# Kernel tuning notes

Hardware: AMD Instinct MI355X
Metric: run time of the kernel (lower is better)

The kernel has to match this reference:

```python
import jax, jax.numpy as jnp
import numpy as np

N_NODES = 50000
N_EDGES = 1600000
IN_F = 512
OUT_F = 256


def setup_inputs() -> dict:
    key = jax.random.key(0)
    k1, k2, k3, k4, k5 = jax.random.split(key, 5)
    features = jax.random.normal(k1, (N_NODES, IN_F), dtype=jnp.float32)
    # xavier_uniform init for weight [in_features, out_features]
    limit = np.sqrt(6.0 / (IN_F + OUT_F)).astype(np.float32)
    weight = jax.random.uniform(k2, (IN_F, OUT_F), dtype=jnp.float32,
                                minval=-limit, maxval=limit)
    # COO sparse adjacency (normalized edge weights in [0,1))
    edge_vals = jax.random.uniform(k3, (N_EDGES,), dtype=jnp.float32)
    edge_rows = jax.random.randint(k4, (N_EDGES,), 0, N_NODES, dtype=jnp.int32)
    edge_cols = jax.random.randint(k5, (N_EDGES,), 0, N_NODES, dtype=jnp.int32)
    return {"features": features, "weight": weight, "edge_vals": edge_vals,
            "edge_rows": edge_rows, "edge_cols": edge_cols}


def reference(features, weight, edge_vals, edge_rows, edge_cols):
    # dropout p=0.0 / eval mode -> identity
    support = features @ weight                      # [N, out_f] dense GEMM
    # torch.spmm(adj, support): out[r] += val * support[c] for each edge (r, c)
    gathered = support[edge_cols] * edge_vals[:, None]   # [E, out_f]
    output = jax.ops.segment_sum(gathered, edge_rows, num_segments=N_NODES)
    return jax.nn.relu(output)
```

## Files before the change

### kernel.cpp

```cpp
#include <hip/hip_runtime.h>

#define N_NODES 50000
#define N_EDGES 1600000
#define IN_F    512
#define OUT_F   256

#define BROWS   128
#define NBINS   ((N_NODES + BROWS - 1) / BROWS)
#define BATCH   2048
#define NBATCHES ((N_EDGES + BATCH - 1) / BATCH)

typedef __attribute__((ext_vector_type(8))) short bf16x8;
typedef __attribute__((ext_vector_type(4))) float f32x4;

__device__ __forceinline__ short bf16rne(float f) {
    unsigned u = __builtin_bit_cast(unsigned, f);
    u += 0x7fffu + ((u >> 16) & 1u);
    return (short)(u >> 16);
}

__device__ __forceinline__ float b2f(unsigned short h) {
    unsigned u = (unsigned)h << 16;
    return __builtin_bit_cast(float, u);
}

__global__ __launch_bounds__(256) void wt_kernel(const float* __restrict__ W,
                                                 short* __restrict__ Wt) {
    int idx = blockIdx.x * 256 + threadIdx.x;
    if (idx < IN_F * OUT_F) {
        int n = idx >> 9;
        int k = idx & 511;
        Wt[idx] = bf16rne(W[(size_t)k * OUT_F + n]);
    }
}

#define ASTRIDE 40
#define BSTRIDE 40

__global__ __launch_bounds__(256) void gemm_mfma_kernel(const float* __restrict__ A,
                                                        const short* __restrict__ Wt,
                                                        unsigned short* __restrict__ Cb) {
    __shared__ short As[64 * ASTRIDE];
    __shared__ short Bs[256 * BSTRIDE];

    const int tid  = threadIdx.x;
    const int wave = tid >> 6;
    const int lane = tid & 63;
    const int m0   = blockIdx.x * 64;
    const int n0w  = wave * 64;

    const int quad = lane >> 4;
    const int l16  = lane & 15;

    const int ar = tid >> 2;
    const int aq = tid & 3;

    f32x4 zero4 = {0.f, 0.f, 0.f, 0.f};
    f32x4 acc[4][4];
#pragma unroll
    for (int i = 0; i < 4; ++i)
#pragma unroll
        for (int j = 0; j < 4; ++j) acc[i][j] = zero4;

    for (int k0 = 0; k0 < IN_F; k0 += 32) {
        {
            const int gm = m0 + ar;
            float4 v0 = make_float4(0.f, 0.f, 0.f, 0.f);
            float4 v1 = v0;
            if (gm < N_NODES) {
                const float* p = A + (size_t)gm * IN_F + k0 + aq * 8;
                v0 = *(const float4*)p;
                v1 = *(const float4*)(p + 4);
            }
            bf16x8 b;
            b[0] = bf16rne(v0.x); b[1] = bf16rne(v0.y);
            b[2] = bf16rne(v0.z); b[3] = bf16rne(v0.w);
            b[4] = bf16rne(v1.x); b[5] = bf16rne(v1.y);
            b[6] = bf16rne(v1.z); b[7] = bf16rne(v1.w);
            *(bf16x8*)&As[ar * ASTRIDE + aq * 8] = b;
        }
        {
            const short* src = Wt + (size_t)tid * IN_F + k0;
            bf16x8 w0 = *(const bf16x8*)(src + 0);
            bf16x8 w1 = *(const bf16x8*)(src + 8);
            bf16x8 w2 = *(const bf16x8*)(src + 16);
            bf16x8 w3 = *(const bf16x8*)(src + 24);
            short* dst = &Bs[tid * BSTRIDE];
            *(bf16x8*)(dst + 0)  = w0;
            *(bf16x8*)(dst + 8)  = w1;
            *(bf16x8*)(dst + 16) = w2;
            *(bf16x8*)(dst + 24) = w3;
        }
        __syncthreads();

        bf16x8 af[4], bf[4];
#pragma unroll
        for (int mt = 0; mt < 4; ++mt)
            af[mt] = *(const bf16x8*)&As[(mt * 16 + l16) * ASTRIDE + quad * 8];
#pragma unroll
        for (int nt = 0; nt < 4; ++nt)
            bf[nt] = *(const bf16x8*)&Bs[(n0w + nt * 16 + l16) * BSTRIDE + quad * 8];

#pragma unroll
        for (int mt = 0; mt < 4; ++mt)
#pragma unroll
            for (int nt = 0; nt < 4; ++nt)
                acc[mt][nt] = __builtin_amdgcn_mfma_f32_16x16x32_bf16(
                    af[mt], bf[nt], acc[mt][nt], 0, 0, 0);
        __syncthreads();
    }

#pragma unroll
    for (int mt = 0; mt < 4; ++mt) {
        const int rbase = m0 + mt * 16 + quad * 4;
#pragma unroll
        for (int i = 0; i < 4; ++i) {
            const int row = rbase + i;
            if (row < N_NODES) {
#pragma unroll
                for (int nt = 0; nt < 4; ++nt)
                    Cb[(size_t)row * OUT_F + n0w + nt * 16 + l16] =
                        (unsigned short)bf16rne(acc[mt][nt][i]);
            }
        }
    }
}

__global__ __launch_bounds__(256) void zero_bins_kernel(int* __restrict__ binCounts) {
    int i = blockIdx.x * 256 + threadIdx.x;
    if (i < NBINS) binCounts[i] = 0;
}

__global__ __launch_bounds__(256) void histA_kernel(const int* __restrict__ rows,
                                                    int* __restrict__ binCounts) {
    __shared__ int lh[NBINS];
    const int tid = threadIdx.x;
    for (int i = tid; i < NBINS; i += 256) lh[i] = 0;
    __syncthreads();
    for (int i = blockIdx.x * 256 + tid; i < N_EDGES; i += gridDim.x * 256)
        atomicAdd(&lh[rows[i] >> 7], 1);
    __syncthreads();
    for (int i = tid; i < NBINS; i += 256)
        if (lh[i]) atomicAdd(&binCounts[i], lh[i]);
}

__global__ __launch_bounds__(256) void scanA_kernel(const int* __restrict__ binCounts,
                                                    int* __restrict__ binStart,
                                                    int* __restrict__ gcursor) {
    __shared__ int stmp[256];
    const int tid = threadIdx.x;
    const int i0 = 2 * tid, i1 = 2 * tid + 1;
    const int a0 = (i0 < NBINS) ? binCounts[i0] : 0;
    const int a1 = (i1 < NBINS) ? binCounts[i1] : 0;
    const int pair = a0 + a1;
    stmp[tid] = pair;
    for (int off = 1; off < 256; off <<= 1) {
        __syncthreads();
        int t = (tid >= off) ? stmp[tid - off] : 0;
        __syncthreads();
        stmp[tid] += t;
    }
    __syncthreads();
    const int pexcl = stmp[tid] - pair;
    if (i0 < NBINS) { binStart[i0] = pexcl;      gcursor[i0] = pexcl; }
    if (i1 < NBINS) { binStart[i1] = pexcl + a0; gcursor[i1] = pexcl + a0; }
}

__global__ __launch_bounds__(256) void fillA_kernel(const int* __restrict__ rows,
                                                    const int* __restrict__ cols,
                                                    const float* __restrict__ vals,
                                                    int* __restrict__ gcursor,
                                                    int2* __restrict__ binned) {
    __shared__ int lhist[NBINS];
    __shared__ int lexcl[NBINS];
    __shared__ int gbase[NBINS];
    __shared__ int stmp[256];
    __shared__ int2 lstage[BATCH];
    __shared__ unsigned short sbucket[BATCH];

    const int tid   = threadIdx.x;
    const int start = blockIdx.x * BATCH;
    const int count = min(BATCH, N_EDGES - start);

    for (int i = tid; i < NBINS; i += 256) lhist[i] = 0;
    __syncthreads();

    int myrow[8], myrank[8];
#pragma unroll
    for (int j = 0; j < 8; ++j) {
        const int s = j * 256 + tid;
        if (s < count) {
            const int r = rows[start + s];
            myrow[j]  = r;
            myrank[j] = atomicAdd(&lhist[r >> 7], 1);
        }
    }
    __syncthreads();

    {
        const int i0 = 2 * tid, i1 = 2 * tid + 1;
        const int a0 = (i0 < NBINS) ? lhist[i0] : 0;
        const int a1 = (i1 < NBINS) ? lhist[i1] : 0;
        const int pair = a0 + a1;
        stmp[tid] = pair;
        for (int off = 1; off < 256; off <<= 1) {
            __syncthreads();
            int t = (tid >= off) ? stmp[tid - off] : 0;
            __syncthreads();
            stmp[tid] += t;
        }
        __syncthreads();
        const int pexcl = stmp[tid] - pair;
        if (i0 < NBINS) {
            lexcl[i0] = pexcl;
            gbase[i0] = a0 ? atomicAdd(&gcursor[i0], a0) : 0;
        }
        if (i1 < NBINS) {
            lexcl[i1] = pexcl + a0;
            gbase[i1] = a1 ? atomicAdd(&gcursor[i1], a1) : 0;
        }
    }
    __syncthreads();

#pragma unroll
    for (int j = 0; j < 8; ++j) {
        const int s = j * 256 + tid;
        if (s < count) {
            const int r   = myrow[j];
            const int b   = r >> 7;
            const int pos = lexcl[b] + myrank[j];
            lstage[pos]  = make_int2(((r & 127) << 16) | cols[start + s],
                                     __float_as_int(vals[start + s]));
            sbucket[pos] = (unsigned short)b;
        }
    }
    __syncthreads();

#pragma unroll
    for (int j = 0; j < 8; ++j) {
        const int s = j * 256 + tid;
        if (s < count) {
            const int b = sbucket[s];
            binned[gbase[b] + (s - lexcl[b])] = lstage[s];
        }
    }
}

__global__ __launch_bounds__(256) void sortB_kernel(const int2* __restrict__ binned,
                                                    const int* __restrict__ binStart,
                                                    const int* __restrict__ binCounts,
                                                    int* __restrict__ excl,
                                                    unsigned int* __restrict__ ecv) {
    __shared__ int lhist[BROWS];
    __shared__ int lcur[BROWS];

    const int tid  = threadIdx.x;
    const int b    = blockIdx.x;
    const int base = binStart[b];
    const int cnt  = binCounts[b];

    if (tid < BROWS) lhist[tid] = 0;
    __syncthreads();

    for (int i = tid; i < cnt; i += 256)
        atomicAdd(&lhist[binned[base + i].x >> 16], 1);
    __syncthreads();

    if (tid < BROWS) lcur[tid] = lhist[tid];
    for (int off = 1; off < BROWS; off <<= 1) {
        __syncthreads();
        int t = (tid >= off && tid < BROWS) ? lcur[tid - off] : 0;
        __syncthreads();
        if (tid < BROWS) lcur[tid] += t;
    }
    __syncthreads();
    if (tid < BROWS) {
        const int pexcl = lcur[tid] - lhist[tid];
        const int row   = b * BROWS + tid;
        lcur[tid] = pexcl;
        if (row < N_NODES) excl[row] = base + pexcl;
    }
    __syncthreads();

    for (int i = tid; i < cnt; i += 256) {
        const int2 e  = binned[base + i];
        const int rl  = e.x >> 16;
        const int col = e.x & 0xFFFF;
        const int rank = atomicAdd(&lcur[rl], 1);
        ecv[base + rank] = ((unsigned int)col << 16) |
                           (unsigned short)bf16rne(__int_as_float(e.y));
    }
}

__global__ __launch_bounds__(256) void gather_kernel(const ushort4* __restrict__ support,
                                                     const int* __restrict__ excl,
                                                     const unsigned int* __restrict__ ecv,
                                                     float4* __restrict__ out) {
    const int tid  = threadIdx.x;
    const int row  = blockIdx.x * 4 + (tid >> 6);
    const int lane = tid & 63;
    if (row >= N_NODES) return;

    const int start = excl[row];
    const int end   = (row + 1 < N_NODES) ? excl[row + 1] : N_EDGES;

    float4 acc = make_float4(0.f, 0.f, 0.f, 0.f);
    int e = start;
    const int end4 = start + ((end - start) & ~3);
    for (; e < end4; e += 4) {
        const unsigned int p0 = ecv[e];
        const unsigned int p1 = ecv[e + 1];
        const unsigned int p2 = ecv[e + 2];
        const unsigned int p3 = ecv[e + 3];
        const ushort4 s0 = support[(size_t)(p0 >> 16) * 64 + lane];
        const ushort4 s1 = support[(size_t)(p1 >> 16) * 64 + lane];
        const ushort4 s2 = support[(size_t)(p2 >> 16) * 64 + lane];
        const ushort4 s3 = support[(size_t)(p3 >> 16) * 64 + lane];
        const float v0 = b2f((unsigned short)(p0 & 0xFFFF));
        const float v1 = b2f((unsigned short)(p1 & 0xFFFF));
        const float v2 = b2f((unsigned short)(p2 & 0xFFFF));
        const float v3 = b2f((unsigned short)(p3 & 0xFFFF));
        acc.x += v0 * b2f(s0.x); acc.y += v0 * b2f(s0.y);
        acc.z += v0 * b2f(s0.z); acc.w += v0 * b2f(s0.w);
        acc.x += v1 * b2f(s1.x); acc.y += v1 * b2f(s1.y);
        acc.z += v1 * b2f(s1.z); acc.w += v1 * b2f(s1.w);
        acc.x += v2 * b2f(s2.x); acc.y += v2 * b2f(s2.y);
        acc.z += v2 * b2f(s2.z); acc.w += v2 * b2f(s2.w);
        acc.x += v3 * b2f(s3.x); acc.y += v3 * b2f(s3.y);
        acc.z += v3 * b2f(s3.z); acc.w += v3 * b2f(s3.w);
    }
    for (; e < end; ++e) {
        const unsigned int p0 = ecv[e];
        const ushort4 s0 = support[(size_t)(p0 >> 16) * 64 + lane];
        const float v0 = b2f((unsigned short)(p0 & 0xFFFF));
        acc.x += v0 * b2f(s0.x); acc.y += v0 * b2f(s0.y);
        acc.z += v0 * b2f(s0.z); acc.w += v0 * b2f(s0.w);
    }

    acc.x = fmaxf(acc.x, 0.f);
    acc.y = fmaxf(acc.y, 0.f);
    acc.z = fmaxf(acc.z, 0.f);
    acc.w = fmaxf(acc.w, 0.f);
    out[(size_t)row * 64 + lane] = acc;
}

extern "C" void kernel_launch(void* const* d_in, const int* in_sizes, int n_in,
                              void* d_out, int out_size, void* d_ws, size_t ws_size,
                              hipStream_t stream) {
    const float* features  = (const float*)d_in[0];
    const float* weight    = (const float*)d_in[1];
    const float* edge_vals = (const float*)d_in[2];
    const int*   edge_rows = (const int*)d_in[3];
    const int*   edge_cols = (const int*)d_in[4];
    float* out = (float*)d_out;

    unsigned short* support_bf = (unsigned short*)d_ws;
    int2*  binned    = (int2*)(support_bf + (size_t)N_NODES * OUT_F);
    unsigned int* ecv = (unsigned int*)(binned + N_EDGES);
    int*   excl      = (int*)(ecv + N_EDGES);
    int*   binCounts = excl + N_NODES;
    int*   binStart  = binCounts + 512;
    int*   gcursor   = binStart + 512;
    short* Wt        = (short*)(gcursor + 512);

    wt_kernel<<<(IN_F * OUT_F + 255) / 256, 256, 0, stream>>>(weight, Wt);

    gemm_mfma_kernel<<<(N_NODES + 63) / 64, 256, 0, stream>>>(features, Wt, support_bf);

    zero_bins_kernel<<<2, 256, 0, stream>>>(binCounts);
    histA_kernel<<<256, 256, 0, stream>>>(edge_rows, binCounts);
    scanA_kernel<<<1, 256, 0, stream>>>(binCounts, binStart, gcursor);
    fillA_kernel<<<NBATCHES, 256, 0, stream>>>(edge_rows, edge_cols, edge_vals,
                                               gcursor, binned);
    sortB_kernel<<<NBINS, 256, 0, stream>>>(binned, binStart, binCounts, excl, ecv);

    gather_kernel<<<(N_NODES + 3) / 4, 256, 0, stream>>>(
        (const ushort4*)support_bf, excl, ecv, (float4*)out);
}
```

Measured before the change: 388.2 us.

## Enlarge GEMM block to 128 rows with 8 waves and split gather launch

The GEMM kernel now uses 512 threads and 128-row tiles, arranged as a 2x4 grid of waves. Each tile of the transposed weight loaded into shared memory is therefore reused across twice as many feature rows, which halves the weight traffic per output row. Separately, the gather kernel takes a row offset and is launched twice over the two halves of the nodes, which adds a launch without any clear benefit. The larger block and its shared memory use could lower occupancy.

```diff
diff --git a/kernel.cpp b/kernel.cpp
--- a/kernel.cpp
+++ b/kernel.cpp
@@ -37,23 +37,27 @@
 #define ASTRIDE 40
 #define BSTRIDE 40
 
-__global__ __launch_bounds__(256) void gemm_mfma_kernel(const float* __restrict__ A,
+__global__ __launch_bounds__(512) void gemm_mfma_kernel(const float* __restrict__ A,
                                                         const short* __restrict__ Wt,
                                                         unsigned short* __restrict__ Cb) {
-    __shared__ short As[64 * ASTRIDE];
+    __shared__ short As[128 * ASTRIDE];
     __shared__ short Bs[256 * BSTRIDE];
 
     const int tid  = threadIdx.x;
     const int wave = tid >> 6;
     const int lane = tid & 63;
-    const int m0   = blockIdx.x * 64;
-    const int n0w  = wave * 64;
+    const int m0   = blockIdx.x * 128;
+    const int wrow = (wave >> 2) * 64;
+    const int wcol = (wave & 3) * 64;
 
     const int quad = lane >> 4;
     const int l16  = lane & 15;
 
     const int ar = tid >> 2;
     const int aq = tid & 3;
+
+    const int bn = tid >> 1;
+    const int bh = tid & 1;
 
     f32x4 zero4 = {0.f, 0.f, 0.f, 0.f};
     f32x4 acc[4][4];
@@ -80,26 +84,22 @@
             *(bf16x8*)&As[ar * ASTRIDE + aq * 8] = b;
         }
         {
-            const short* src = Wt + (size_t)tid * IN_F + k0;
+            const short* src = Wt + (size_t)bn * IN_F + k0 + bh * 16;
             bf16x8 w0 = *(const bf16x8*)(src + 0);
             bf16x8 w1 = *(const bf16x8*)(src + 8);
-            bf16x8 w2 = *(const bf16x8*)(src + 16);
-            bf16x8 w3 = *(const bf16x8*)(src + 24);
-            short* dst = &Bs[tid * BSTRIDE];
-            *(bf16x8*)(dst + 0)  = w0;
-            *(bf16x8*)(dst + 8)  = w1;
-            *(bf16x8*)(dst + 16) = w2;
-            *(bf16x8*)(dst + 24) = w3;
+            short* dst = &Bs[bn * BSTRIDE + bh * 16];
+            *(bf16x8*)(dst + 0) = w0;
+            *(bf16x8*)(dst + 8) = w1;
         }
         __syncthreads();
 
         bf16x8 af[4], bf[4];
 #pragma unroll
         for (int mt = 0; mt < 4; ++mt)
-            af[mt] = *(const bf16x8*)&As[(mt * 16 + l16) * ASTRIDE + quad * 8];
+            af[mt] = *(const bf16x8*)&As[(wrow + mt * 16 + l16) * ASTRIDE + quad * 8];
 #pragma unroll
         for (int nt = 0; nt < 4; ++nt)
-            bf[nt] = *(const bf16x8*)&Bs[(n0w + nt * 16 + l16) * BSTRIDE + quad * 8];
+            bf[nt] = *(const bf16x8*)&Bs[(wcol + nt * 16 + l16) * BSTRIDE + quad * 8];
 
 #pragma unroll
         for (int mt = 0; mt < 4; ++mt)
@@ -112,14 +112,14 @@
 
 #pragma unroll
     for (int mt = 0; mt < 4; ++mt) {
-        const int rbase = m0 + mt * 16 + quad * 4;
+        const int rbase = m0 + wrow + mt * 16 + quad * 4;
 #pragma unroll
         for (int i = 0; i < 4; ++i) {
             const int row = rbase + i;
             if (row < N_NODES) {
 #pragma unroll
                 for (int nt = 0; nt < 4; ++nt)
-                    Cb[(size_t)row * OUT_F + n0w + nt * 16 + l16] =
+                    Cb[(size_t)row * OUT_F + wcol + nt * 16 + l16] =
                         (unsigned short)bf16rne(acc[mt][nt][i]);
             }
         }
@@ -295,9 +295,10 @@
 __global__ __launch_bounds__(256) void gather_kernel(const ushort4* __restrict__ support,
                                                      const int* __restrict__ excl,
                                                      const unsigned int* __restrict__ ecv,
-                                                     float4* __restrict__ out) {
+                                                     float4* __restrict__ out,
+                                                     int row0) {
     const int tid  = threadIdx.x;
-    const int row  = blockIdx.x * 4 + (tid >> 6);
+    const int row  = row0 + blockIdx.x * 4 + (tid >> 6);
     const int lane = tid & 63;
     if (row >= N_NODES) return;
 
@@ -365,7 +366,7 @@
 
     wt_kernel<<<(IN_F * OUT_F + 255) / 256, 256, 0, stream>>>(weight, Wt);
 
-    gemm_mfma_kernel<<<(N_NODES + 63) / 64, 256, 0, stream>>>(features, Wt, support_bf);
+    gemm_mfma_kernel<<<(N_NODES + 127) / 128, 512, 0, stream>>>(features, Wt, support_bf);
 
     zero_bins_kernel<<<2, 256, 0, stream>>>(binCounts);
     histA_kernel<<<256, 256, 0, stream>>>(edge_rows, binCounts);
@@ -374,6 +375,8 @@
                                                gcursor, binned);
     sortB_kernel<<<NBINS, 256, 0, stream>>>(binned, binStart, binCounts, excl, ecv);
 
-    gather_kernel<<<(N_NODES + 3) / 4, 256, 0, stream>>>(
-        (const ushort4*)support_bf, excl, ecv, (float4*)out);
-}
+    gather_kernel<<<25000 / 4, 256, 0, stream>>>(
+        (const ushort4*)support_bf, excl, ecv, (float4*)out, 0);
+    gather_kernel<<<25000 / 4, 256, 0, stream>>>(
+        (const ushort4*)support_bf, excl, ecv, (float4*)out, 25000);
+}
```

Measured after the change: 373.0 us. 3.9% less time.
